# Performance work log

Hardware: AMD Instinct MI355X
Metric: run time of the kernel (lower is better)

## Reference

```python
import jax, jax.numpy as jnp
import numpy as np

DIM = 1024      # internal_dim
HEADS = 16
HD = DIM // HEADS
M = 256         # meaning_dim (protected prefix)
E = 4           # num_experts
K = 2           # top_k
HID = 2048      # dim * ffn_mult
MID = 2048      # DeepNarrow mid = 2*dim
LB = 0.01
EPS = 1.1920929e-07  # torch.finfo(float32).eps (nn.RMSNorm default)


def _rms(x, w):
    return x * jax.lax.rsqrt(jnp.mean(x * x, axis=-1, keepdims=True) + EPS) * w


def _gelu(x):
    return jax.nn.gelu(x, approximate=False)  # F.gelu default (erf)


def setup_inputs() -> dict:
    key = jax.random.key(0)
    ks = jax.random.split(key, 20)
    d = DIM
    w = lambda k, s: (jax.random.normal(k, s, jnp.float32) * 0.02)
    return {
        "x": jax.random.normal(ks[0], (4, 1024, d), jnp.float32),
        "n1_w": jnp.ones((d,), jnp.float32),
        "n2_w": jnp.ones((d,), jnp.float32),
        "wq": w(ks[1], (d, d)), "wk": w(ks[2], (d, d)),
        "wv": w(ks[3], (d, d)), "wo": w(ks[4], (d, d)),
        "qn_w": jnp.ones((HD,), jnp.float32), "kn_w": jnp.ones((HD,), jnp.float32),
        "gate_w": w(ks[5], (E, d)),
        # expert 0: StandardFFN
        "e0_up": w(ks[6], (HID, d)), "e0_down": w(ks[7], (d, HID)),
        # expert 1: SwiGLUFFN
        "e1_w1": w(ks[8], (HID, d)), "e1_w2": w(ks[9], (HID, d)), "e1_down": w(ks[10], (d, HID)),
        # expert 2: DeepNarrowFFN
        "e2_l1": w(ks[11], (MID, d)), "e2_l2": w(ks[12], (HID, MID)),
        "e2_l3": w(ks[13], (MID, HID)), "e2_l4": w(ks[14], (d, MID)),
        # expert 3: BottleneckFFN (neck = dim)
        "e3_down": w(ks[15], (d, d)), "e3_up": w(ks[16], (HID, d)), "e3_out": w(ks[17], (d, HID)),
    }


def reference(x, n1_w, n2_w, wq, wk, wv, wo, qn_w, kn_w, gate_w,
              e0_up, e0_down, e1_w1, e1_w2, e1_down,
              e2_l1, e2_l2, e2_l3, e2_l4, e3_down, e3_up, e3_out):
    B, T, C = x.shape
    # ---- attention with QK-norm, causal (NoPE) ----
    h = _rms(x, n1_w)
    heads = lambda w_: (h @ w_.T).reshape(B, T, HEADS, HD).transpose(0, 2, 1, 3)  # [B,H,T,hd]
    q = _rms(heads(wq), qn_w)
    k = _rms(heads(wk), kn_w)
    v = heads(wv)
    scores = jnp.einsum('bhqd,bhkd->bhqk', q, k) * (HD ** -0.5)
    causal = jnp.tril(jnp.ones((T, T), bool))
    scores = jnp.where(causal[None, None], scores, -jnp.inf)
    attn = jax.nn.softmax(scores, axis=-1)
    ao = jnp.einsum('bhqk,bhkd->bhqd', attn, v).transpose(0, 2, 1, 3).reshape(B, T, C) @ wo.T
    ao = ao.at[:, :, :M].set(0.0)  # protect meaning dims
    x = x + ao
    # ---- heterogeneous MoE, top-k routing ----
    xf = _rms(x, n2_w).reshape(-1, C)  # [N,C]
    N = xf.shape[0]
    logits = jnp.nan_to_num(xf @ gate_w.T)
    probs = jax.nn.softmax(logits, axis=-1)
    topv, topi = jax.lax.top_k(probs, K)
    topv = topv / (topv.sum(-1, keepdims=True) + 1e-8)
    # dense per-token combine weights: zero for unselected experts (same math as dispatch loop)
    wts = jnp.zeros((N, E), x.dtype).at[jnp.arange(N)[:, None], topi].add(topv)
    o0 = _gelu(xf @ e0_up.T) @ e0_down.T
    o1 = (jax.nn.silu(xf @ e1_w1.T) * (xf @ e1_w2.T)) @ e1_down.T
    o2 = _gelu(_gelu(_gelu(xf @ e2_l1.T) @ e2_l2.T) @ e2_l3.T) @ e2_l4.T
    o3 = _gelu(_gelu(xf @ e3_down.T) @ e3_up.T) @ e3_out.T
    moe = (wts[:, 0:1] * o0 + wts[:, 1:2] * o1 + wts[:, 2:3] * o2 + wts[:, 3:4] * o3)
    moe = moe.reshape(B, T, C).at[:, :, :M].set(0.0)
    return x + moe
```

## Files before the change

### kernel.cpp

```cpp
#include <hip/hip_runtime.h>
#include <math.h>

#define DIM   1024
#define NTOK  4096
#define TSEQ  1024
#define NHEAD 16
#define MPROT 256
#define EPSR  1.1920929e-07f
#define SA    64.0f
#define SW    256.0f
#define SPC   64.0f
#define MAXI  160

typedef __attribute__((ext_vector_type(8))) short          short8;
typedef __attribute__((ext_vector_type(8))) _Float16       half8;
typedef __attribute__((ext_vector_type(4))) _Float16       half4;
typedef __attribute__((ext_vector_type(4))) float          f32x4;
typedef __attribute__((ext_vector_type(4))) unsigned short us4;

static __device__ __forceinline__ float bf2f(unsigned short s) {
  union { unsigned int u; float f; } c; c.u = ((unsigned int)s) << 16; return c.f;
}
static __device__ __forceinline__ unsigned short f2bf(float f) {
  union { float f; unsigned int u; } c; c.f = f;
  return (unsigned short)((c.u + 0x7fffu + ((c.u >> 16) & 1u)) >> 16);
}
static __device__ __forceinline__ void gload16(void* lds, const void* g) {
  __builtin_amdgcn_global_load_lds(
      (__attribute__((address_space(1))) void*)const_cast<void*>(g),
      (__attribute__((address_space(3))) void*)lds, 16, 0, 0);
}

static __device__ __forceinline__ void tile_swz(int& m0, int& n0) {
  const int gx = gridDim.x;
  const int L = blockIdx.y * gx + blockIdx.x;
  const int xcd = L & 7;
  const int j = L >> 3;
  const int mbq = j / gx;
  const int nb = j - mbq * gx;
  m0 = ((mbq << 3) | xcd) << 7;
  n0 = nb << 7;
}

__global__ __launch_bounds__(256) void cvt_attn4_k(const float* __restrict__ wq,
                                                   const float* __restrict__ wk,
                                                   const float* __restrict__ wv,
                                                   const float* __restrict__ wo,
                                                   _Float16* __restrict__ dh,
                                                   _Float16* __restrict__ dl) {
  const int wi = blockIdx.y;
  const float* s = (wi == 0) ? wq : (wi == 1) ? wk : (wi == 2) ? wv : wo;
  const int i = blockIdx.x * 256 + threadIdx.x;
  const size_t off4 = ((size_t)wi << 20) >> 2;
  const float4 v = ((const float4*)s)[i];
  float a0 = v.x * SW, a1 = v.y * SW, a2 = v.z * SW, a3 = v.w * SW;
  half4 hv, lv;
  _Float16 h0 = (_Float16)a0; hv[0] = h0; lv[0] = (_Float16)(a0 - (float)h0);
  _Float16 h1 = (_Float16)a1; hv[1] = h1; lv[1] = (_Float16)(a1 - (float)h1);
  _Float16 h2 = (_Float16)a2; hv[2] = h2; lv[2] = (_Float16)(a2 - (float)h2);
  _Float16 h3 = (_Float16)a3; hv[3] = h3; lv[3] = (_Float16)(a3 - (float)h3);
  ((half4*)dh)[off4 + i] = hv; ((half4*)dl)[off4 + i] = lv;
}

__global__ __launch_bounds__(256) void cvt_moe_all_k(
    const float* s0, const float* s1, const float* s2, const float* s3,
    const float* s4, const float* s5, const float* s6, const float* s7,
    const float* s8, const float* s9, const float* s10, const float* s11,
    unsigned short* __restrict__ dst) {
  const int n4tab[12] = {524288, 524288, 524288, 524288, 524288, 524288,
                         1048576, 1048576, 524288, 262144, 524288, 524288};
  const size_t offtab[12] = {0, 2097152, 4194304, 6291456, 8388608, 10485760,
                             12582912, 16777216, 20971520, 23068672, 24117248, 26214400};
  const int wi = blockIdx.y;
  const int i = blockIdx.x * 256 + threadIdx.x;
  if (i >= n4tab[wi]) return;
  const float* s;
  switch (wi) {
    case 0: s = s0; break; case 1: s = s1; break; case 2: s = s2; break;
    case 3: s = s3; break; case 4: s = s4; break; case 5: s = s5; break;
    case 6: s = s6; break; case 7: s = s7; break; case 8: s = s8; break;
    case 9: s = s9; break; case 10: s = s10; break; default: s = s11; break;
  }
  const float4 v = ((const float4*)s)[i];
  us4 o; o[0] = f2bf(v.x); o[1] = f2bf(v.y); o[2] = f2bf(v.z); o[3] = f2bf(v.w);
  ((us4*)(dst + offtab[wi]))[i] = o;
}

__global__ __launch_bounds__(256) void rms_split_k(const float* __restrict__ in,
                                                   const float* __restrict__ wgt,
                                                   _Float16* __restrict__ oh,
                                                   _Float16* __restrict__ ol) {
  const int row = blockIdx.x, tid = threadIdx.x;
  const float4 v = ((const float4*)(in + (size_t)row * DIM))[tid];
  float ss = v.x * v.x + v.y * v.y + v.z * v.z + v.w * v.w;
#pragma unroll
  for (int o = 32; o; o >>= 1) ss += __shfl_xor(ss, o);
  __shared__ float red[4];
  if ((tid & 63) == 0) red[tid >> 6] = ss;
  __syncthreads();
  const float sc = rsqrtf((red[0] + red[1] + red[2] + red[3]) * (1.0f / DIM) + EPSR) * SA;
  const float4 wv = ((const float4*)wgt)[tid];
  float a[4] = {v.x * sc * wv.x, v.y * sc * wv.y, v.z * sc * wv.z, v.w * sc * wv.w};
  half4 hv, lv;
#pragma unroll
  for (int j = 0; j < 4; ++j) {
    _Float16 hh = (_Float16)a[j]; hv[j] = hh; lv[j] = (_Float16)(a[j] - (float)hh);
  }
  ((half4*)(oh + (size_t)row * DIM))[tid] = hv;
  ((half4*)(ol + (size_t)row * DIM))[tid] = lv;
}

__global__ __launch_bounds__(256) void rmsgate_k(const float* __restrict__ x2,
                                                 const float* __restrict__ n2w,
                                                 const float* __restrict__ gw,
                                                 unsigned short* __restrict__ xfb,
                                                 float* __restrict__ wts) {
  const int row = blockIdx.x, tid = threadIdx.x;
  const float4 v = ((const float4*)(x2 + (size_t)row * DIM))[tid];
  float ss = v.x * v.x + v.y * v.y + v.z * v.z + v.w * v.w;
#pragma unroll
  for (int o = 32; o; o >>= 1) ss += __shfl_xor(ss, o);
  __shared__ float red[4];
  __shared__ float redE[4][4];
  const int w = tid >> 6, lane = tid & 63;
  if (lane == 0) red[w] = ss;
  __syncthreads();
  const float sc = rsqrtf((red[0] + red[1] + red[2] + red[3]) * (1.0f / DIM) + EPSR);
  const float4 nw = ((const float4*)n2w)[tid];
  const float xn0 = v.x * sc * nw.x, xn1 = v.y * sc * nw.y;
  const float xn2 = v.z * sc * nw.z, xn3 = v.w * sc * nw.w;
  us4 ob; ob[0] = f2bf(xn0); ob[1] = f2bf(xn1); ob[2] = f2bf(xn2); ob[3] = f2bf(xn3);
  ((us4*)(xfb + (size_t)row * DIM))[tid] = ob;
#pragma unroll
  for (int e = 0; e < 4; ++e) {
    const float4 g = ((const float4*)(gw + (size_t)e * DIM))[tid];
    float d = xn0 * g.x + xn1 * g.y + xn2 * g.z + xn3 * g.w;
#pragma unroll
    for (int o = 32; o; o >>= 1) d += __shfl_xor(d, o);
    if (lane == 0) redE[w][e] = d;
  }
  __syncthreads();
  if (tid == 0) {
    float lg[4];
#pragma unroll
    for (int e = 0; e < 4; ++e) lg[e] = redE[0][e] + redE[1][e] + redE[2][e] + redE[3][e];
    const float mx = fmaxf(fmaxf(lg[0], lg[1]), fmaxf(lg[2], lg[3]));
    float pe[4]; float sum = 0.0f;
#pragma unroll
    for (int e = 0; e < 4; ++e) { pe[e] = __expf(lg[e] - mx); sum += pe[e]; }
#pragma unroll
    for (int e = 0; e < 4; ++e) pe[e] /= sum;
    int i1 = 0;
    for (int e = 1; e < 4; ++e) if (pe[e] > pe[i1]) i1 = e;
    int i2 = -1;
    for (int e = 0; e < 4; ++e) { if (e == i1) continue; if (i2 < 0 || pe[e] > pe[i2]) i2 = e; }
    const float s2 = pe[i1] + pe[i2] + 1e-8f;
    float o[4] = {0.f, 0.f, 0.f, 0.f};
    o[i1] = pe[i1] / s2; o[i2] = pe[i2] / s2;
    float4 r; r.x = o[0]; r.y = o[1]; r.z = o[2]; r.w = o[3];
    *(float4*)(wts + (size_t)row * 4) = r;
  }
}

struct MoeCfg { int nbn[4][4]; int ks[4][4]; };

__global__ __launch_bounds__(256) void route2_k(const float* __restrict__ wts,
                                                int* __restrict__ idxP,
                                                int* __restrict__ meta,
                                                int* __restrict__ work,
                                                MoeCfg cfg) {
  const int tid = threadIdx.x, w = tid >> 6, lane = tid & 63;
  __shared__ int wsum[4];
  __shared__ int baseS;
  int off = 0;
  for (int e = 0; e < 4; ++e) {
    if (tid == 0) baseS = 0;
    __syncthreads();
    for (int c = 0; c < 16; ++c) {
      const int tok = (c << 8) + tid;
      const bool pred = wts[(size_t)tok * 4 + e] > 0.0f;
      const unsigned long long m = __ballot(pred);
      const int lanepre = __popcll(m & ((1ull << lane) - 1ull));
      if (lane == 0) wsum[w] = __popcll(m);
      __syncthreads();
      int wpre = 0;
#pragma unroll
      for (int i = 0; i < 4; ++i) wpre += (i < w) ? wsum[i] : 0;
      const int tot = wsum[0] + wsum[1] + wsum[2] + wsum[3];
      if (pred) idxP[off + baseS + wpre + lanepre] = tok;
      __syncthreads();
      if (tid == 0) baseS += tot;
      __syncthreads();
    }
    const int cnt = baseS;
    const int padded = (cnt + 127) & ~127;
    for (int j = cnt + tid; j < padded; j += 256) idxP[off + j] = -1;
    if (tid == 0) meta[80 + e] = off;
    const int mb0 = off >> 7, nmb = padded >> 7;
    for (int j = tid; j < nmb; j += 256) meta[mb0 + j] = e;
    off += padded;
    __syncthreads();
  }
  for (int j = (off >> 7) + tid; j < 72; j += 256) meta[j] = -1;
  for (int j = tid; j < 4 * 8 * MAXI; j += 256) work[j] = -1;
  __syncthreads();
  if (tid < 32) {
    const int p = tid >> 3, x = tid & 7;
    int* wb = work + p * (8 * MAXI);
    int n = 0;
    const int totmb = off >> 7;
    for (int mb = x; mb < totmb; mb += 8) {
      const int e = meta[mb];
      const int nbn = cfg.nbn[p][e];
      const int ks = cfg.ks[p][e];
      for (int nb = 0; nb < nbn; ++nb)
        for (int k = 0; k < ks; ++k) {
          wb[n * 8 + x] = mb | (nb << 8) | (k << 16);
          ++n;
        }
    }
  }
}

struct SubOpP {
  const unsigned short* A;
  const unsigned short* Bw;
  unsigned short* outb;
  const unsigned short* other;
  int K, nbn, act, ep, gath, ks;
};
struct PhaseP { SubOpP op[4]; };

__global__ __launch_bounds__(256, 4) void gemm_moe_k(PhaseP ph,
                                                     const int* __restrict__ meta,
                                                     const int* __restrict__ idxP,
                                                     const float* __restrict__ wts,
                                                     float* __restrict__ outp,
                                                     const int* __restrict__ wk) {
  __shared__ unsigned short As[128][64];
  __shared__ unsigned short Bs[128][64];
  const int item = wk[blockIdx.y * 8 + blockIdx.x];
  if (item < 0) return;
  const int mb = item & 255;
  const int nb = (item >> 8) & 255;
  const int kpart = (item >> 16) & 3;
  const int e = meta[mb];
  SubOpP op;
  switch (e) {
    case 0: op = ph.op[0]; break;
    case 1: op = ph.op[1]; break;
    case 2: op = ph.op[2]; break;
    default: op = ph.op[3]; break;
  }
  const int m0p = mb << 7;
  const int lr0 = m0p - meta[80 + e];
  const int n0 = nb << 7;
  const int F = op.nbn << 7;
  const int K = op.K;
  const int tid = threadIdx.x;
  const int w = tid >> 6, lane = tid & 63;
  const int wr = ((w >> 1) << 6), wc = ((w & 1) << 6);
  const int rr = lane & 15, kgl = lane >> 4;
  const int srow = tid >> 3, sslot = tid & 7;

  int grow[4];
#pragma unroll
  for (int i = 0; i < 4; ++i) {
    const int r = (i << 5) + srow;
    if (op.gath) {
      const int t = idxP[m0p + r];
      grow[i] = (t < 0) ? 0 : t;
    } else {
      grow[i] = lr0 + r;
    }
  }

  f32x4 acc[4][4];
#pragma unroll
  for (int a_ = 0; a_ < 4; ++a_)
#pragma unroll
    for (int b_ = 0; b_ < 4; ++b_) acc[a_][b_] = (f32x4){0.f, 0.f, 0.f, 0.f};

  int kt0 = 0, ktN = K >> 6;
  if (op.ks == 2) { const int hgt = ktN >> 1; kt0 = kpart * hgt; ktN = kt0 + hgt; }
  for (int kt = kt0; kt < ktN; ++kt) {
    const int k0 = kt << 6;
#pragma unroll
    for (int i = 0; i < 4; ++i) {
      const int r = (i << 5) + srow;
      const int ls = sslot ^ (r & 7);
      gload16(&As[(i << 5) + (w << 3)][0], op.A + (size_t)grow[i] * K + k0 + (ls << 3));
      gload16(&Bs[(i << 5) + (w << 3)][0], op.Bw + (size_t)(n0 + r) * K + k0 + (ls << 3));
    }
    __syncthreads();
    short8 af[4][2], bfr[4][2];
#pragma unroll
    for (int f = 0; f < 4; ++f) {
#pragma unroll
      for (int ks = 0; ks < 2; ++ks) {
        const int row = wr + (f << 4) + rr;
        const int kg = (ks << 2) + kgl;
        af[f][ks] = *(const short8*)&As[row][(kg ^ (row & 7)) << 3];
        const int col = wc + (f << 4) + rr;
        bfr[f][ks] = *(const short8*)&Bs[col][(kg ^ (col & 7)) << 3];
      }
    }
#pragma unroll
    for (int fi = 0; fi < 4; ++fi)
#pragma unroll
      for (int fj = 0; fj < 4; ++fj)
#pragma unroll
        for (int ks = 0; ks < 2; ++ks)
          acc[fi][fj] = __builtin_amdgcn_mfma_f32_16x16x32_bf16(
              af[fi][ks], bfr[fj][ks], acc[fi][fj], 0, 0, 0);
    __syncthreads();
  }
#pragma unroll
  for (int fi = 0; fi < 4; ++fi)
#pragma unroll
    for (int fj = 0; fj < 4; ++fj) {
      const int col = n0 + wc + (fj << 4) + rr;
#pragma unroll
      for (int r = 0; r < 4; ++r) {
        const int rl = wr + (fi << 4) + (kgl << 2) + r;
        float v = acc[fi][fj][r];
        if (op.act) v = 0.5f * v * (1.0f + erff(v * 0.70710678118654752f));
        if (op.ep == 0) {
          op.outb[(size_t)(lr0 + rl) * F + col] = f2bf(v);
        } else if (op.ep == 1) {
          const size_t off = (size_t)(lr0 + rl) * F + col;
          const float sv = v / (1.0f + __expf(-v));
          op.outb[off] = f2bf(sv * bf2f(op.other[off]));
        } else {
          const int tok = idxP[m0p + rl];
          if (tok >= 0 && col >= MPROT)
            atomicAdd(&outp[(size_t)tok * DIM + col], wts[(size_t)tok * 4 + e] * v);
        }
      }
    }
}

template <int EP>
__global__ __launch_bounds__(256, 4) void gemm_split_k(
    const _Float16* __restrict__ Ah, const _Float16* __restrict__ Al,
    const _Float16* __restrict__ Bh, const _Float16* __restrict__ Bl,
    int K, int F,
    _Float16* __restrict__ Oh, _Float16* __restrict__ Ol, float oscale,
    const float* __restrict__ resid, float* __restrict__ outf,
    _Float16* __restrict__ K2h, _Float16* __restrict__ K2l,
    _Float16* __restrict__ V2h, _Float16* __restrict__ V2l,
    const float* __restrict__ qnw, const float* __restrict__ knw) {
  __shared__ _Float16 AsH[128][32], AsL[128][32];
  __shared__ _Float16 BsH[128][32], BsL[128][32];
  const int tid = threadIdx.x;
  const int w = tid >> 6, lane = tid & 63;
  const int wr = ((w >> 1) << 6), wc = ((w & 1) << 6);
  int m0, n0;
  tile_swz(m0, n0);
  const int rr = lane & 15, kgl = lane >> 4;
  const int srow = tid >> 2, sslot = tid & 3;

  f32x4 acc[4][4];
#pragma unroll
  for (int a_ = 0; a_ < 4; ++a_)
#pragma unroll
    for (int b_ = 0; b_ < 4; ++b_) acc[a_][b_] = (f32x4){0.f, 0.f, 0.f, 0.f};

  const int KT = K >> 5;
  for (int kt = 0; kt < KT; ++kt) {
    const int k0 = kt << 5;
#pragma unroll
    for (int i = 0; i < 2; ++i) {
      const int r = (i << 6) + srow;
      const int ls = sslot ^ ((r >> 1) & 3);
      const size_t ga = (size_t)(m0 + r) * K + k0 + (ls << 3);
      const size_t gb = (size_t)(n0 + r) * K + k0 + (ls << 3);
      const int lr = (i << 6) + (w << 4);
      gload16(&AsH[lr][0], Ah + ga);
      gload16(&AsL[lr][0], Al + ga);
      gload16(&BsH[lr][0], Bh + gb);
      gload16(&BsL[lr][0], Bl + gb);
    }
    __syncthreads();
    half8 ah[4], al[4], bh[4], bl[4];
#pragma unroll
    for (int f = 0; f < 4; ++f) {
      const int row = wr + (f << 4) + rr;
      const int pa = (kgl ^ ((row >> 1) & 3)) << 3;
      ah[f] = *(const half8*)&AsH[row][pa];
      al[f] = *(const half8*)&AsL[row][pa];
      const int col = wc + (f << 4) + rr;
      const int pb = (kgl ^ ((col >> 1) & 3)) << 3;
      bh[f] = *(const half8*)&BsH[col][pb];
      bl[f] = *(const half8*)&BsL[col][pb];
    }
#pragma unroll
    for (int fi = 0; fi < 4; ++fi)
#pragma unroll
      for (int fj = 0; fj < 4; ++fj) {
        acc[fi][fj] = __builtin_amdgcn_mfma_f32_16x16x32_f16(ah[fi], bh[fj], acc[fi][fj], 0, 0, 0);
        acc[fi][fj] = __builtin_amdgcn_mfma_f32_16x16x32_f16(ah[fi], bl[fj], acc[fi][fj], 0, 0, 0);
        acc[fi][fj] = __builtin_amdgcn_mfma_f32_16x16x32_f16(al[fi], bh[fj], acc[fi][fj], 0, 0, 0);
      }
    __syncthreads();
  }

  if (EP == 3 && n0 < 2048) {
    const bool isq = (n0 < 1024);
    _Float16* ph = isq ? Oh : K2h;
    _Float16* pl = isq ? Ol : K2l;
    const float* wvec = isq ? qnw : knw;
    float wreg[4];
#pragma unroll
    for (int fj = 0; fj < 4; ++fj) wreg[fj] = wvec[(fj << 4) + rr];
#pragma unroll
    for (int fi = 0; fi < 4; ++fi) {
#pragma unroll
      for (int r = 0; r < 4; ++r) {
        float vv[4]; float ss = 0.f;
#pragma unroll
        for (int fj = 0; fj < 4; ++fj) {
          vv[fj] = acc[fi][fj][r] * oscale;
          ss += vv[fj] * vv[fj];
        }
        ss += __shfl_xor(ss, 1);
        ss += __shfl_xor(ss, 2);
        ss += __shfl_xor(ss, 4);
        ss += __shfl_xor(ss, 8);
        const float sc = rsqrtf(ss * (1.0f / (64.0f * SA * SA)) + EPSR);
        const int row = m0 + wr + (fi << 4) + (kgl << 2) + r;
#pragma unroll
        for (int fj = 0; fj < 4; ++fj) {
          const int c = (n0 + wc + (fj << 4) + rr) & 1023;
          const float nv = vv[fj] * sc * wreg[fj];
          const _Float16 hh2 = (_Float16)nv;
          const size_t off = (size_t)row * DIM + c;
          ph[off] = hh2; pl[off] = (_Float16)(nv - (float)hh2);
        }
      }
    }
    return;
  }

#pragma unroll
  for (int fi = 0; fi < 4; ++fi)
#pragma unroll
    for (int fj = 0; fj < 4; ++fj) {
      const int col = n0 + wc + (fj << 4) + rr;
      const int rowb = m0 + wr + (fi << 4) + (kgl << 2);
      if (EP == 3) {
        const int c2 = col - 2048;
        half4 h4, l4;
#pragma unroll
        for (int r = 0; r < 4; ++r) {
          const float v = acc[fi][fj][r] * oscale;
          const _Float16 hh2 = (_Float16)v;
          h4[r] = hh2; l4[r] = (_Float16)(v - (float)hh2);
        }
        const size_t vt = ((size_t)((rowb >> 10) << 4) + (size_t)(c2 >> 6)) * 65536 +
                          (size_t)(c2 & 63) * 1024 + (size_t)(rowb & 1023);
        *(half4*)&V2h[vt] = h4;
        *(half4*)&V2l[vt] = l4;
      } else {
#pragma unroll
        for (int r = 0; r < 4; ++r) {
          const size_t off = (size_t)(rowb + r) * F + col;
          const float v = acc[fi][fj][r] * oscale;
          outf[off] = resid[off] + (col >= MPROT ? v : 0.0f);
        }
      }
    }
}

__global__ __launch_bounds__(256, 2) void attn_k(
    const _Float16* __restrict__ Qh, const _Float16* __restrict__ Ql,
    const _Float16* __restrict__ Kh, const _Float16* __restrict__ Kl,
    const _Float16* __restrict__ Vth, const _Float16* __restrict__ Vtl,
    _Float16* __restrict__ Oh, _Float16* __restrict__ Ol) {
  __shared__ _Float16 Ksh[2][32][64], Ksl[2][32][64];
  __shared__ _Float16 Vsh[2][64][40], Vsl[2][64][40];
  __shared__ _Float16 Plh[4][16][40], Pll[4][16][40];
  const int n = blockIdx.x;
  const int j = n >> 1, s = n & 1;
  const int pt = j >> 6;
  const int qt = s ? (7 - pt) : pt;
  const int bh = j & 63;
  const int b = bh >> 4, h = bh & 15;
  const int tid = threadIdx.x, w = tid >> 6, lane = tid & 63;
  const int rr = lane & 15, rg = lane >> 4;
  const size_t tokbase = (size_t)b * TSEQ;
  const int hcol = h << 6;
  const size_t vtbase = (size_t)bh << 16;
  const int q0w = (qt << 7) + (w << 5);
  const float sscale = 0.125f / (SA * SA);

  half8 qfh[2][2], qfl[2][2];
#pragma unroll
  for (int qf = 0; qf < 2; ++qf)
#pragma unroll
    for (int ks = 0; ks < 2; ++ks) {
      const size_t off = (tokbase + q0w + (qf << 4) + rr) * DIM + hcol + (ks << 5) + (rg << 3);
      qfh[qf][ks] = *(const half8*)&Qh[off];
      qfl[qf][ks] = *(const half8*)&Ql[off];
    }

  f32x4 oacc[2][4];
#pragma unroll
  for (int qf = 0; qf < 2; ++qf)
#pragma unroll
    for (int dg = 0; dg < 4; ++dg) oacc[qf][dg] = (f32x4){0.f, 0.f, 0.f, 0.f};
  float mreg[2] = {-INFINITY, -INFINITY}, lreg[2] = {0.f, 0.f};

  const int kr = (w << 3) + (lane >> 3);
  const int kswz = ((lane & 7) ^ (kr & 7)) << 3;
  const int vr = tid >> 2;
  const int vs = (tid & 3) << 3;

  const int ntiles = (qt + 1) << 2;

  {
    gload16(&Ksh[0][w << 3][0], &Kh[(tokbase + kr) * DIM + hcol + kswz]);
    gload16(&Ksl[0][w << 3][0], &Kl[(tokbase + kr) * DIM + hcol + kswz]);
    const half8 vvh = *(const half8*)&Vth[vtbase + (size_t)vr * TSEQ + vs];
    const half8 vvl = *(const half8*)&Vtl[vtbase + (size_t)vr * TSEQ + vs];
    *(half8*)&Vsh[0][vr][vs] = vvh;
    *(half8*)&Vsl[0][vr][vs] = vvl;
    __syncthreads();
  }

  for (int t = 0; t < ntiles; ++t) {
    const int cur = t & 1;
    const int kv0 = t << 5;
    const bool havenext = (t + 1 < ntiles);
    half8 nvh, nvl;
    if (havenext) {
      const int kn = kv0 + 32;
      gload16(&Ksh[cur ^ 1][w << 3][0], &Kh[(tokbase + kn + kr) * DIM + hcol + kswz]);
      gload16(&Ksl[cur ^ 1][w << 3][0], &Kl[(tokbase + kn + kr) * DIM + hcol + kswz]);
      nvh = *(const half8*)&Vth[vtbase + (size_t)vr * TSEQ + kn + vs];
      nvl = *(const half8*)&Vtl[vtbase + (size_t)vr * TSEQ + kn + vs];
    }
    if (kv0 <= q0w + 31) {
      half8 kfh[2][2], kfl[2][2];
#pragma unroll
      for (int kt = 0; kt < 2; ++kt)
#pragma unroll
        for (int ks = 0; ks < 2; ++ks) {
          const int row = (kt << 4) + rr;
          const int sw = ((((ks << 2) + rg)) ^ (row & 7)) << 3;
          kfh[kt][ks] = *(const half8*)&Ksh[cur][row][sw];
          kfl[kt][ks] = *(const half8*)&Ksl[cur][row][sw];
        }
#pragma unroll
      for (int qf = 0; qf < 2; ++qf) {
        if (kv0 > q0w + (qf << 4) + 15) continue;
        f32x4 st[2];
        st[0] = (f32x4){0.f, 0.f, 0.f, 0.f};
        st[1] = (f32x4){0.f, 0.f, 0.f, 0.f};
        __builtin_amdgcn_s_setprio(1);
#pragma unroll
        for (int kt = 0; kt < 2; ++kt)
#pragma unroll
          for (int ks = 0; ks < 2; ++ks) {
            st[kt] = __builtin_amdgcn_mfma_f32_16x16x32_f16(kfh[kt][ks], qfh[qf][ks], st[kt], 0, 0, 0);
            st[kt] = __builtin_amdgcn_mfma_f32_16x16x32_f16(kfh[kt][ks], qfl[qf][ks], st[kt], 0, 0, 0);
            st[kt] = __builtin_amdgcn_mfma_f32_16x16x32_f16(kfl[kt][ks], qfh[qf][ks], st[kt], 0, 0, 0);
          }
        __builtin_amdgcn_s_setprio(0);
        const int qg = q0w + (qf << 4) + rr;
        float s2[2][4]; float mx = -INFINITY;
#pragma unroll
        for (int kt = 0; kt < 2; ++kt)
#pragma unroll
          for (int r = 0; r < 4; ++r) {
            float sv = st[kt][r] * sscale;
            if (kv0 + (kt << 4) + (rg << 2) + r > qg) sv = -INFINITY;
            s2[kt][r] = sv; mx = fmaxf(mx, sv);
          }
        mx = fmaxf(mx, __shfl_xor(mx, 16));
        mx = fmaxf(mx, __shfl_xor(mx, 32));
        const float mn = fmaxf(mreg[qf], mx);
        const float al = __expf(mreg[qf] - mn);
        mreg[qf] = mn;
        float p[2][4]; float rs = 0.f;
#pragma unroll
        for (int kt = 0; kt < 2; ++kt)
#pragma unroll
          for (int r = 0; r < 4; ++r) { p[kt][r] = __expf(s2[kt][r] - mn); rs += p[kt][r]; }
        rs += __shfl_xor(rs, 16);
        rs += __shfl_xor(rs, 32);
        lreg[qf] = lreg[qf] * al + rs;
#pragma unroll
        for (int kt = 0; kt < 2; ++kt) {
          half4 h4, l4;
#pragma unroll
          for (int r = 0; r < 4; ++r) {
            const float pv = p[kt][r] * SPC;
            const _Float16 ph = (_Float16)pv;
            h4[r] = ph; l4[r] = (_Float16)(pv - (float)ph);
          }
          *(half4*)&Plh[w][rr][(kt << 4) + (rg << 2)] = h4;
          *(half4*)&Pll[w][rr][(kt << 4) + (rg << 2)] = l4;
        }
        float alr[4];
#pragma unroll
        for (int r = 0; r < 4; ++r) alr[r] = __shfl(al, (lane & 48) | ((rg << 2) + r));
#pragma unroll
        for (int dg = 0; dg < 4; ++dg)
#pragma unroll
          for (int r = 0; r < 4; ++r) oacc[qf][dg][r] *= alr[r];
        const half8 pah = *(const half8*)&Plh[w][rr][rg << 3];
        const half8 pal = *(const half8*)&Pll[w][rr][rg << 3];
        __builtin_amdgcn_s_setprio(1);
#pragma unroll
        for (int dg = 0; dg < 4; ++dg) {
          const half8 vfh2 = *(const half8*)&Vsh[cur][(dg << 4) + rr][rg << 3];
          const half8 vfl2 = *(const half8*)&Vsl[cur][(dg << 4) + rr][rg << 3];
          oacc[qf][dg] = __builtin_amdgcn_mfma_f32_16x16x32_f16(pah, vfh2, oacc[qf][dg], 0, 0, 0);
          oacc[qf][dg] = __builtin_amdgcn_mfma_f32_16x16x32_f16(pah, vfl2, oacc[qf][dg], 0, 0, 0);
          oacc[qf][dg] = __builtin_amdgcn_mfma_f32_16x16x32_f16(pal, vfh2, oacc[qf][dg], 0, 0, 0);
        }
        __builtin_amdgcn_s_setprio(0);
      }
    }
    if (havenext) {
      *(half8*)&Vsh[cur ^ 1][vr][vs] = nvh;
      *(half8*)&Vsl[cur ^ 1][vr][vs] = nvl;
    }
    __syncthreads();
  }
#pragma unroll
  for (int qf = 0; qf < 2; ++qf) {
    float li[4];
#pragma unroll
    for (int r = 0; r < 4; ++r)
      li[r] = __shfl(lreg[qf], (lane & 48) | ((rg << 2) + r));
#pragma unroll
    for (int dg = 0; dg < 4; ++dg)
#pragma unroll
      for (int r = 0; r < 4; ++r) {
        const int qloc = (rg << 2) + r;
        const float ov = oacc[qf][dg][r] / (li[r] * SPC);
        const _Float16 hh2 = (_Float16)ov;
        const size_t off = (tokbase + q0w + (qf << 4) + qloc) * DIM + hcol + (dg << 4) + rr;
        Oh[off] = hh2;
        Ol[off] = (_Float16)(ov - (float)hh2);
      }
  }
}

extern "C" void kernel_launch(void* const* d_in, const int* in_sizes, int n_in,
                              void* d_out, int out_size, void* d_ws, size_t ws_size,
                              hipStream_t stream) {
  (void)in_sizes; (void)n_in; (void)out_size; (void)ws_size;
  const float* x    = (const float*)d_in[0];
  const float* n1w  = (const float*)d_in[1];
  const float* n2w  = (const float*)d_in[2];
  const float* wq   = (const float*)d_in[3];
  const float* wk   = (const float*)d_in[4];
  const float* wv   = (const float*)d_in[5];
  const float* wo   = (const float*)d_in[6];
  const float* qnw  = (const float*)d_in[7];
  const float* knw  = (const float*)d_in[8];
  const float* gw   = (const float*)d_in[9];
  const float* moesrc[12] = {
    (const float*)d_in[10], (const float*)d_in[11],
    (const float*)d_in[12], (const float*)d_in[13], (const float*)d_in[14],
    (const float*)d_in[15], (const float*)d_in[16], (const float*)d_in[17], (const float*)d_in[18],
    (const float*)d_in[19], (const float*)d_in[20], (const float*)d_in[21]
  };
  float* outp = (float*)d_out;

  char* p = (char*)d_ws;
  auto alloc = [&](size_t bytes) { void* r = (void*)p; p += (bytes + 255) & ~(size_t)255; return r; };
  const size_t NC = (size_t)NTOK * DIM;
  _Float16* hh = (_Float16*)alloc(NC * 2);
  _Float16* hl = (_Float16*)alloc(NC * 2);
  _Float16* qh = (_Float16*)alloc(NC * 2);
  _Float16* ql = (_Float16*)alloc(NC * 2);
  _Float16* kh = (_Float16*)alloc(NC * 2);
  _Float16* kl = (_Float16*)alloc(NC * 2);
  _Float16* vth = (_Float16*)alloc(NC * 2);
  _Float16* vtl = (_Float16*)alloc(NC * 2);
  unsigned short* xfb = (unsigned short*)alloc(NC * 2);
  float* wts = (float*)alloc((size_t)NTOK * 4 * 4);
  _Float16* awh = (_Float16*)alloc((size_t)4 * 1024 * 1024 * 2);
  _Float16* awl = (_Float16*)alloc((size_t)4 * 1024 * 1024 * 2);
  unsigned short* moeW = (unsigned short*)alloc((size_t)28311552 * 2);
  int* idxP = (int*)alloc((size_t)9216 * 4);
  int* meta = (int*)alloc(512);
  int* work = (int*)alloc((size_t)4 * 8 * MAXI * 4);
  unsigned short* e0t = (unsigned short*)qh;
  unsigned short* e1a = (unsigned short*)kh;
  unsigned short* e2a = (unsigned short*)vth;
  unsigned short* e1b = (unsigned short*)alloc((size_t)NTOK * 2048 * 2);
  unsigned short* e2b = (unsigned short*)alloc((size_t)NTOK * 2048 * 2);
  unsigned short* e3a = (unsigned short*)alloc((size_t)NTOK * 1024 * 2);
  unsigned short* e3b = (unsigned short*)alloc((size_t)NTOK * 2048 * 2);
  unsigned short* e2c = e2a;

  const size_t moff[12] = {0, 2097152, 4194304, 6291456, 8388608, 10485760,
                           12582912, 16777216, 20971520, 23068672, 24117248, 26214400};
  auto mw = [&](int i) -> const unsigned short* { return moeW + moff[i]; };

  cvt_attn4_k<<<dim3(1024, 4), dim3(256), 0, stream>>>(wq, wk, wv, wo, awh, awl);
  cvt_moe_all_k<<<dim3(4096, 12), dim3(256), 0, stream>>>(
      moesrc[0], moesrc[1], moesrc[2], moesrc[3], moesrc[4], moesrc[5],
      moesrc[6], moesrc[7], moesrc[8], moesrc[9], moesrc[10], moesrc[11], moeW);
  const _Float16* woh = awh + (3 << 20); const _Float16* wol = awl + (3 << 20);

  rms_split_k<<<dim3(NTOK), dim3(256), 0, stream>>>(x, n1w, hh, hl);
  gemm_split_k<3><<<dim3(24, 32), dim3(256), 0, stream>>>(
      hh, hl, awh, awl, 1024, 3072, qh, ql, 1.0f / SW, nullptr, nullptr,
      kh, kl, vth, vtl, qnw, knw);
  attn_k<<<dim3(512), dim3(256), 0, stream>>>(qh, ql, kh, kl, vth, vtl, hh, hl);
  gemm_split_k<1><<<dim3(8, 32), dim3(256), 0, stream>>>(
      hh, hl, woh, wol, 1024, 1024, nullptr, nullptr, 1.0f / (SA * SW), x, outp,
      nullptr, nullptr, nullptr, nullptr, nullptr, nullptr);

  rmsgate_k<<<dim3(NTOK), dim3(256), 0, stream>>>(outp, n2w, gw, xfb, wts);

  MoeCfg cfg;
  const int nbn_tab[4][4] = {{16, 16, 16, 8},
                             {8, 16, 16, 16},
                             {0, 8, 16, 0},
                             {0, 0, 8, 8}};
  const int ks_tab[4][4]  = {{1, 1, 1, 1},
                             {2, 1, 1, 1},
                             {1, 2, 1, 1},
                             {1, 1, 2, 2}};
  for (int pp = 0; pp < 4; ++pp)
    for (int ee = 0; ee < 4; ++ee) { cfg.nbn[pp][ee] = nbn_tab[pp][ee]; cfg.ks[pp][ee] = ks_tab[pp][ee]; }

  route2_k<<<dim3(1), dim3(256), 0, stream>>>(wts, idxP, meta, work, cfg);

  auto mk = [&](const unsigned short* A, const unsigned short* B, unsigned short* outb,
                const unsigned short* other, int K, int nbn, int act, int ep, int gath, int ks) {
    SubOpP s; s.A = A; s.Bw = B; s.outb = outb; s.other = other;
    s.K = K; s.nbn = nbn; s.act = act; s.ep = ep; s.gath = gath; s.ks = ks;
    return s;
  };
  const SubOpP none = mk(nullptr, nullptr, nullptr, nullptr, 1024, 0, 0, 0, 0, 1);

  PhaseP p1;
  p1.op[0] = mk(xfb, mw(0), e0t, nullptr, 1024, 16, 1, 0, 1, 1);
  p1.op[1] = mk(xfb, mw(3), e1a, nullptr, 1024, 16, 0, 0, 1, 1);
  p1.op[2] = mk(xfb, mw(5), e2a, nullptr, 1024, 16, 1, 0, 1, 1);
  p1.op[3] = mk(xfb, mw(9), e3a, nullptr, 1024, 8, 1, 0, 1, 1);
  gemm_moe_k<<<dim3(8, MAXI), dim3(256), 0, stream>>>(p1, meta, idxP, wts, outp, work);

  PhaseP p2;
  p2.op[0] = mk(e0t, mw(1), nullptr, nullptr, 2048, 8, 0, 2, 0, 2);
  p2.op[1] = mk(xfb, mw(2), e1b, e1a, 1024, 16, 0, 1, 1, 1);
  p2.op[2] = mk(e2a, mw(6), e2b, nullptr, 2048, 16, 1, 0, 0, 1);
  p2.op[3] = mk(e3a, mw(10), e3b, nullptr, 1024, 16, 1, 0, 0, 1);
  gemm_moe_k<<<dim3(8, MAXI), dim3(256), 0, stream>>>(p2, meta, idxP, wts, outp, work + 8 * MAXI);

  PhaseP p3;
  p3.op[0] = none;
  p3.op[1] = mk(e1b, mw(4), nullptr, nullptr, 2048, 8, 0, 2, 0, 2);
  p3.op[2] = mk(e2b, mw(7), e2c, nullptr, 2048, 16, 1, 0, 0, 1);
  p3.op[3] = none;
  gemm_moe_k<<<dim3(8, MAXI), dim3(256), 0, stream>>>(p3, meta, idxP, wts, outp, work + 16 * MAXI);

  PhaseP p4;
  p4.op[0] = none;
  p4.op[1] = none;
  p4.op[2] = mk(e2c, mw(8), nullptr, nullptr, 2048, 8, 0, 2, 0, 2);
  p4.op[3] = mk(e3b, mw(11), nullptr, nullptr, 2048, 8, 0, 2, 0, 2);
  gemm_moe_k<<<dim3(8, MAXI), dim3(256), 0, stream>>>(p4, meta, idxP, wts, outp, work + 24 * MAXI);
}
```

Measured before the change: 596.3 us.

## Double-buffer MoE GEMM LDS tiles and split-K the output projection

The MoE GEMM gets double-buffered shared-memory tiles so the next K tile is loaded while the current one is multiplied, and launch bounds drop from 4 to 2 blocks per CU to fit the doubled LDS. The output-projection GEMM is split along K across two z-blocks. Each split atomically adds its partial into an output buffer that is first filled with the residual by an async device copy. This targets load latency and low grid occupancy (256 blocks) in the output projection, at the cost of fewer resident MoE blocks, extra atomics, a memcpy, and a nondeterministic summation order.

```diff
diff --git a/kernel.cpp b/kernel.cpp
--- a/kernel.cpp
+++ b/kernel.cpp
@@ -231,14 +231,14 @@
 };
 struct PhaseP { SubOpP op[4]; };
 
-__global__ __launch_bounds__(256, 4) void gemm_moe_k(PhaseP ph,
+__global__ __launch_bounds__(256, 2) void gemm_moe_k(PhaseP ph,
                                                      const int* __restrict__ meta,
                                                      const int* __restrict__ idxP,
                                                      const float* __restrict__ wts,
                                                      float* __restrict__ outp,
                                                      const int* __restrict__ wk) {
-  __shared__ unsigned short As[128][64];
-  __shared__ unsigned short Bs[128][64];
+  __shared__ unsigned short As[2][128][64];
+  __shared__ unsigned short Bs[2][128][64];
   const int item = wk[blockIdx.y * 8 + blockIdx.x];
   if (item < 0) return;
   const int mb = item & 255;
@@ -283,16 +283,22 @@
 
   int kt0 = 0, ktN = K >> 6;
   if (op.ks == 2) { const int hgt = ktN >> 1; kt0 = kpart * hgt; ktN = kt0 + hgt; }
-  for (int kt = kt0; kt < ktN; ++kt) {
+
+  auto stage = [&](int buf, int kt) {
     const int k0 = kt << 6;
 #pragma unroll
     for (int i = 0; i < 4; ++i) {
       const int r = (i << 5) + srow;
       const int ls = sslot ^ (r & 7);
-      gload16(&As[(i << 5) + (w << 3)][0], op.A + (size_t)grow[i] * K + k0 + (ls << 3));
-      gload16(&Bs[(i << 5) + (w << 3)][0], op.Bw + (size_t)(n0 + r) * K + k0 + (ls << 3));
-    }
-    __syncthreads();
+      gload16(&As[buf][(i << 5) + (w << 3)][0], op.A + (size_t)grow[i] * K + k0 + (ls << 3));
+      gload16(&Bs[buf][(i << 5) + (w << 3)][0], op.Bw + (size_t)(n0 + r) * K + k0 + (ls << 3));
+    }
+  };
+  stage(0, kt0);
+  __syncthreads();
+  for (int kt = kt0; kt < ktN; ++kt) {
+    const int cur = (kt - kt0) & 1;
+    if (kt + 1 < ktN) stage(cur ^ 1, kt + 1);
     short8 af[4][2], bfr[4][2];
 #pragma unroll
     for (int f = 0; f < 4; ++f) {
@@ -300,9 +306,9 @@
       for (int ks = 0; ks < 2; ++ks) {
         const int row = wr + (f << 4) + rr;
         const int kg = (ks << 2) + kgl;
-        af[f][ks] = *(const short8*)&As[row][(kg ^ (row & 7)) << 3];
+        af[f][ks] = *(const short8*)&As[cur][row][(kg ^ (row & 7)) << 3];
         const int col = wc + (f << 4) + rr;
-        bfr[f][ks] = *(const short8*)&Bs[col][(kg ^ (col & 7)) << 3];
+        bfr[f][ks] = *(const short8*)&Bs[cur][col][(kg ^ (col & 7)) << 3];
       }
     }
 #pragma unroll
@@ -346,7 +352,7 @@
     const _Float16* __restrict__ Bh, const _Float16* __restrict__ Bl,
     int K, int F,
     _Float16* __restrict__ Oh, _Float16* __restrict__ Ol, float oscale,
-    const float* __restrict__ resid, float* __restrict__ outf,
+    float* __restrict__ outf,
     _Float16* __restrict__ K2h, _Float16* __restrict__ K2l,
     _Float16* __restrict__ V2h, _Float16* __restrict__ V2l,
     const float* __restrict__ qnw, const float* __restrict__ knw) {
@@ -366,8 +372,9 @@
 #pragma unroll
     for (int b_ = 0; b_ < 4; ++b_) acc[a_][b_] = (f32x4){0.f, 0.f, 0.f, 0.f};
 
-  const int KT = K >> 5;
-  for (int kt = 0; kt < KT; ++kt) {
+  int kt0 = 0, ktN = K >> 5;
+  if (EP == 1) { const int hgt = ktN >> 1; kt0 = blockIdx.z * hgt; ktN = kt0 + hgt; }
+  for (int kt = kt0; kt < ktN; ++kt) {
     const int k0 = kt << 5;
 #pragma unroll
     for (int i = 0; i < 2; ++i) {
@@ -462,11 +469,12 @@
         *(half4*)&V2h[vt] = h4;
         *(half4*)&V2l[vt] = l4;
       } else {
-#pragma unroll
-        for (int r = 0; r < 4; ++r) {
-          const size_t off = (size_t)(rowb + r) * F + col;
-          const float v = acc[fi][fj][r] * oscale;
-          outf[off] = resid[off] + (col >= MPROT ? v : 0.0f);
+        if (col >= MPROT) {
+#pragma unroll
+          for (int r = 0; r < 4; ++r) {
+            const size_t off = (size_t)(rowb + r) * F + col;
+            atomicAdd(&outf[off], acc[fi][fj][r] * oscale);
+          }
         }
       }
     }
@@ -711,11 +719,12 @@
 
   rms_split_k<<<dim3(NTOK), dim3(256), 0, stream>>>(x, n1w, hh, hl);
   gemm_split_k<3><<<dim3(24, 32), dim3(256), 0, stream>>>(
-      hh, hl, awh, awl, 1024, 3072, qh, ql, 1.0f / SW, nullptr, nullptr,
+      hh, hl, awh, awl, 1024, 3072, qh, ql, 1.0f / SW, nullptr,
       kh, kl, vth, vtl, qnw, knw);
   attn_k<<<dim3(512), dim3(256), 0, stream>>>(qh, ql, kh, kl, vth, vtl, hh, hl);
-  gemm_split_k<1><<<dim3(8, 32), dim3(256), 0, stream>>>(
-      hh, hl, woh, wol, 1024, 1024, nullptr, nullptr, 1.0f / (SA * SW), x, outp,
+  hipMemcpyAsync(outp, x, NC * sizeof(float), hipMemcpyDeviceToDevice, stream);
+  gemm_split_k<1><<<dim3(8, 32, 2), dim3(256), 0, stream>>>(
+      hh, hl, woh, wol, 1024, 1024, nullptr, nullptr, 1.0f / (SA * SW), outp,
       nullptr, nullptr, nullptr, nullptr, nullptr, nullptr);
 
   rmsgate_k<<<dim3(NTOK), dim3(256), 0, stream>>>(outp, n2w, gw, xfb, wts);
```

Result: slower. 677.0 us (+13.5%).
